# Optimization experiments

Hardware: AMD Instinct MI355X
Metric: run time of the kernel (lower is better)

## Reference

```python
import jax, jax.numpy as jnp
import numpy as np

D_MODEL = 1024
HEADS = 16
D_K = D_MODEL // HEADS
D_FF = 4096
EPS = 1e-5


def _layernorm(x, gamma, beta):
    mu = jnp.mean(x, axis=-1, keepdims=True)
    var = jnp.var(x, axis=-1, keepdims=True)
    return (x - mu) * jax.lax.rsqrt(var + EPS) * gamma + beta


def setup_inputs() -> dict:
    key = jax.random.key(0)
    ks = jax.random.split(key, 8)
    s = 0.02
    return {
        "x": jax.random.normal(ks[0], (4, 2048, D_MODEL), dtype=jnp.float32),
        "wq": jax.random.normal(ks[1], (D_MODEL, D_MODEL), dtype=jnp.float32) * s,
        "wk": jax.random.normal(ks[2], (D_MODEL, D_MODEL), dtype=jnp.float32) * s,
        "wv": jax.random.normal(ks[3], (D_MODEL, D_MODEL), dtype=jnp.float32) * s,
        "wo": jax.random.normal(ks[4], (D_MODEL, D_MODEL), dtype=jnp.float32) * s,
        "w1": jax.random.normal(ks[5], (D_MODEL, D_FF), dtype=jnp.float32) * s,
        "b1": jnp.zeros((D_FF,), dtype=jnp.float32),
        "w2": jax.random.normal(ks[6], (D_FF, D_MODEL), dtype=jnp.float32) * s,
        "b2": jnp.zeros((D_MODEL,), dtype=jnp.float32),
        "g1": jnp.ones((D_MODEL,), dtype=jnp.float32),
        "be1": jnp.zeros((D_MODEL,), dtype=jnp.float32),
        "g2": jnp.ones((D_MODEL,), dtype=jnp.float32),
        "be2": jnp.zeros((D_MODEL,), dtype=jnp.float32),
    }


def reference(x, wq, wk, wv, wo, w1, b1, w2, b2, g1, be1, g2, be2):
    B, S, D = x.shape
    # --- multi-head self-attention (dropout = identity at eval) ---
    q = (x @ wq).reshape(B, S, HEADS, D_K).transpose(0, 2, 1, 3)  # [B,H,S,dk]
    k = (x @ wk).reshape(B, S, HEADS, D_K).transpose(0, 2, 1, 3)
    v = (x @ wv).reshape(B, S, HEADS, D_K).transpose(0, 2, 1, 3)
    scores = jnp.einsum("bhqd,bhkd->bhqk", q, k) / jnp.sqrt(jnp.float32(D_K))
    attn = jax.nn.softmax(scores, axis=-1)
    ctx = jnp.einsum("bhqk,bhkd->bhqd", attn, v)
    ctx = ctx.transpose(0, 2, 1, 3).reshape(B, S, D)
    attn_out = ctx @ wo
    # --- add & norm 1 ---
    h = _layernorm(x + attn_out, g1, be1)
    # --- FFN ---
    ffn = jax.nn.relu(h @ w1 + b1) @ w2 + b2
    # --- add & norm 2 ---
    return _layernorm(h + ffn, g2, be2)
```

## Files before the change

kernel.cpp:

```cpp
#include <hip/hip_runtime.h>
#include <hip/hip_bf16.h>


typedef float  floatx2  __attribute__((ext_vector_type(2)));
typedef float  floatx4  __attribute__((ext_vector_type(4)));
typedef float  floatx16 __attribute__((ext_vector_type(16)));
typedef short  shortx8  __attribute__((ext_vector_type(8)));
typedef short  shortx4  __attribute__((ext_vector_type(4)));
typedef int    intx4    __attribute__((ext_vector_type(4)));
typedef unsigned uintx2 __attribute__((ext_vector_type(2)));

__device__ __forceinline__ short f2bs(float f) {
    union { float f; unsigned u; } a; a.f = f;
    unsigned r = a.u + 0x7fffu + ((a.u >> 16) & 1u);
    return (short)(r >> 16);
}

__device__ __forceinline__ float fexp2(float x) {
#if __has_builtin(__builtin_amdgcn_exp2f)
    return __builtin_amdgcn_exp2f(x);
#else
    return __expf(0.6931471805599453f * x);
#endif
}

__device__ __forceinline__ void lane32swap(unsigned& a, unsigned& b) {
#if __has_builtin(__builtin_amdgcn_permlane32_swap)
    uintx2 r = __builtin_amdgcn_permlane32_swap(a, b, false, false);
    a = r[0]; b = r[1];
#else
    int hl = (threadIdx.x & 63) >> 5;
    unsigned ta = (unsigned)__shfl_xor((int)a, 32);
    unsigned tb = (unsigned)__shfl_xor((int)b, 32);
    unsigned na = hl ? tb : a;
    unsigned nb = hl ? b : ta;
    a = na; b = nb;
#endif
}

__device__ __forceinline__ void gload16(const short* g, short* l) {
    __builtin_amdgcn_global_load_lds(
        (const __attribute__((address_space(1))) void*)g,
        (__attribute__((address_space(3))) void*)l,
        16, 0, 0);
}

#define WAITV(n) asm volatile("s_waitcnt vmcnt(" #n ")" ::: "memory")
#define FENCE    asm volatile("" ::: "memory")

__device__ __forceinline__ void trans_tile(const float* __restrict__ in,
                                           short* __restrict__ out,
                                           int N, int K, int k0, int n0,
                                           short (*t)[68]) {
    const int tid = threadIdx.x;
    const int r = tid >> 4, c4 = (tid & 15) * 4;
#pragma unroll
    for (int i = 0; i < 4; ++i) {
        int k = r + i * 16;
        floatx4 v = *(const floatx4*)(in + (size_t)(k0 + k) * N + n0 + c4);
        shortx4 s;
#pragma unroll
        for (int j = 0; j < 4; ++j) s[j] = f2bs(v[j]);
        *(shortx4*)(&t[k][c4]) = s;
    }
    __syncthreads();
#pragma unroll
    for (int i = 0; i < 4; ++i) {
        int n = r + i * 16;
        shortx4 s;
#pragma unroll
        for (int j = 0; j < 4; ++j) s[j] = t[c4 + j][n];
        *(shortx4*)(out + (size_t)(n0 + n) * K + k0 + c4) = s;
    }
}

__global__ __launch_bounds__(256) void prep_kernel(
    const float* __restrict__ wq, const float* __restrict__ wk,
    const float* __restrict__ wv, const float* __restrict__ wo,
    const float* __restrict__ w1, const float* __restrict__ w2,
    const float* __restrict__ x,
    short* wqt, short* wkt, short* wvt, short* wot,
    short* w1t, short* w2t, short* xb)
{
    __shared__ __align__(16) short t[64][68];
    const int bid = blockIdx.x;
    if (bid < 1024) {
        const int widx = bid >> 8, local = bid & 255;
        const float* in = widx == 0 ? wq : widx == 1 ? wk : widx == 2 ? wv : wo;
        short* out = widx == 0 ? wqt : widx == 1 ? wkt : widx == 2 ? wvt : wot;
        trans_tile(in, out, 1024, 1024, (local & 15) * 64, (local >> 4) * 64, t);
    } else if (bid < 2048) {
        const int local = bid - 1024;
        trans_tile(w1, w1t, 4096, 1024, (local & 15) * 64, (local >> 4) * 64, t);
    } else if (bid < 3072) {
        const int local = bid - 2048;
        trans_tile(w2, w2t, 1024, 4096, (local & 63) * 64, (local >> 6) * 64, t);
    } else {
        const int local = bid - 3072;
#pragma unroll
        for (int j = 0; j < 4; ++j) {
            int i = local * 1024 + j * 256 + threadIdx.x;
            floatx4 v = *(const floatx4*)(x + (size_t)i * 4);
            shortx4 o;
            o[0] = f2bs(v[0]); o[1] = f2bs(v[1]); o[2] = f2bs(v[2]); o[3] = f2bs(v[3]);
            *(shortx4*)(xb + (size_t)i * 4) = o;
        }
    }
}

template<int EPI, int BN>
__global__ __launch_bounds__(512, 2) void gemm256(
    const short* __restrict__ A, const short* __restrict__ Bt, const int K, const int N,
    short* __restrict__ outb, float* __restrict__ outf,
    const float* __restrict__ bias, const float* __restrict__ resf)
{
    constexpr int BUFSZ = 16384 + BN * 64;
    constexpr int NF = BN / 64;
    constexpr int NBUF = (BN == 128) ? 3 : 2;
    __shared__ __align__(16) short Ls[NBUF * BUFSZ];
    const int tid = threadIdx.x;
    const int w = tid >> 6, lane = tid & 63;
    const int quad = lane >> 4, l16 = lane & 15;
    const int wm = w >> 2, wn = w & 3;
    const int bx = blockIdx.x, by = blockIdx.y;

    const int srow = w * 16 + (lane >> 3);
    const int uc0 = ((lane & 7) ^ ((lane >> 4) & 7)) * 8;
    const int uc1 = ((lane & 7) ^ (((lane >> 4) + 4) & 7)) * 8;
    const short* aS0 = A  + (size_t)(by * 256 + srow) * K + uc0;
    const short* aS1 = A  + (size_t)(by * 256 + srow + 8) * K + uc1;
    const short* bS0 = Bt + (size_t)(bx * BN + srow) * K + uc0;
    const short* bS1 = Bt + (size_t)(bx * BN + srow + 8) * K + uc1;
    const size_t hK = (size_t)128 * K;
    const int wsl = w * 1024;

    const int rswz = (l16 >> 1) & 7;
    const int ru0 = (quad ^ rswz) * 8;
    const int ru1 = ((4 + quad) ^ rswz) * 8;
    const int aRd = (wm * 64 + l16) * 64;
    const int bRd = (wn * 32 + l16) * 64;

    floatx4 acc[8][NF] = {};
    shortx8 af[4][2], blo[2][2], bhi[2][2];

#define S_A0(buf, kc) { short* p = Ls + (buf) * BUFSZ + wsl;         gload16(aS0 + (kc), p);      gload16(aS1 + (kc), p + 512);      FENCE; }
#define S_A1(buf, kc) { short* p = Ls + (buf) * BUFSZ + 8192 + wsl;  gload16(aS0 + hK + (kc), p); gload16(aS1 + hK + (kc), p + 512); FENCE; }
#define S_B0(buf, kc) { short* p = Ls + (buf) * BUFSZ + 16384 + wsl; gload16(bS0 + (kc), p);      gload16(bS1 + (kc), p + 512);      FENCE; }
#define S_B1(buf, kc) { short* p = Ls + (buf) * BUFSZ + 24576 + wsl; gload16(bS0 + hK + (kc), p); gload16(bS1 + hK + (kc), p + 512); FENCE; }
#define MF(a, b, c) c = __builtin_amdgcn_mfma_f32_16x16x32_bf16(a, b, c, 0, 0, 0)

#define RD_ALO(Ab) {                                                      \
_Pragma("unroll")                                                         \
        for (int mf = 0; mf < 4; ++mf) {                                  \
            af[mf][0] = *(const shortx8*)((Ab) + aRd + mf * 1024 + ru0);  \
            af[mf][1] = *(const shortx8*)((Ab) + aRd + mf * 1024 + ru1);  \
        } }
#define RD_AHI(Ab) {                                                      \
_Pragma("unroll")                                                         \
        for (int mf = 0; mf < 4; ++mf) {                                  \
            af[mf][0] = *(const shortx8*)((Ab) + aRd + 8192 + mf * 1024 + ru0); \
            af[mf][1] = *(const shortx8*)((Ab) + aRd + 8192 + mf * 1024 + ru1); \
        } }
#define RD_BLO(Bb) {                                                      \
_Pragma("unroll")                                                         \
        for (int nf = 0; nf < 2; ++nf) {                                  \
            blo[nf][0] = *(const shortx8*)((Bb) + bRd + nf * 1024 + ru0); \
            blo[nf][1] = *(const shortx8*)((Bb) + bRd + nf * 1024 + ru1); \
        } }
#define MFMA_LO { __builtin_amdgcn_s_setprio(1);                          \
_Pragma("unroll")                                                         \
        for (int mf = 0; mf < 4; ++mf)                                    \
_Pragma("unroll")                                                         \
            for (int nf = 0; nf < 2; ++nf) {                              \
                MF(af[mf][0], blo[nf][0], acc[mf][nf]);                   \
                MF(af[mf][1], blo[nf][1], acc[mf][nf]);                   \
            }                                                             \
        __builtin_amdgcn_s_setprio(0); }
#define MFMA_HI { __builtin_amdgcn_s_setprio(1);                          \
_Pragma("unroll")                                                         \
        for (int mf = 0; mf < 4; ++mf)                                    \
_Pragma("unroll")                                                         \
            for (int nf = 0; nf < 2; ++nf) {                              \
                MF(af[mf][0], blo[nf][0], acc[4 + mf][nf]);               \
                MF(af[mf][1], blo[nf][1], acc[4 + mf][nf]);               \
            }                                                             \
        __builtin_amdgcn_s_setprio(0); }

    const int NT = K >> 6;

    if constexpr (BN == 256) {
        S_A0(0, 0) S_B0(0, 0) S_B1(0, 0) S_A1(0, 0)
        for (int t = 0; t < NT - 1; ++t) {
            const int rb = t & 1, wbuf = rb ^ 1, kc = (t + 1) * 64;
            const short* Ab = Ls + rb * BUFSZ;
            const short* Bb = Ab + 16384;
            WAITV(4); __builtin_amdgcn_s_barrier(); FENCE;
            RD_ALO(Ab) RD_BLO(Bb)
            S_A0(wbuf, kc)
            MFMA_LO
            WAITV(4); __builtin_amdgcn_s_barrier(); FENCE;
#pragma unroll
            for (int nf = 0; nf < 2; ++nf) {
                bhi[nf][0] = *(const shortx8*)(Bb + bRd + 8192 + nf * 1024 + ru0);
                bhi[nf][1] = *(const shortx8*)(Bb + bRd + 8192 + nf * 1024 + ru1);
            }
            S_B0(wbuf, kc)
            __builtin_amdgcn_s_setprio(1);
#pragma unroll
            for (int mf = 0; mf < 4; ++mf)
#pragma unroll
                for (int nf = 0; nf < 2; ++nf) {
                    MF(af[mf][0], bhi[nf][0], acc[mf][2 + nf]);
                    MF(af[mf][1], bhi[nf][1], acc[mf][2 + nf]);
                }
            __builtin_amdgcn_s_setprio(0);
            WAITV(4); __builtin_amdgcn_s_barrier(); FENCE;
            RD_AHI(Ab)
            S_B1(wbuf, kc)
            MFMA_HI
            S_A1(wbuf, kc)
            __builtin_amdgcn_s_setprio(1);
#pragma unroll
            for (int mf = 0; mf < 4; ++mf)
#pragma unroll
                for (int nf = 0; nf < 2; ++nf) {
                    MF(af[mf][0], bhi[nf][0], acc[4 + mf][2 + nf]);
                    MF(af[mf][1], bhi[nf][1], acc[4 + mf][2 + nf]);
                }
            __builtin_amdgcn_s_setprio(0);
        }
        {
            const int rb = (NT - 1) & 1;
            const short* Ab = Ls + rb * BUFSZ;
            const short* Bb = Ab + 16384;
            WAITV(4); __builtin_amdgcn_s_barrier(); FENCE;
            RD_ALO(Ab) RD_BLO(Bb)
            MFMA_LO
            WAITV(2); __builtin_amdgcn_s_barrier(); FENCE;
#pragma unroll
            for (int nf = 0; nf < 2; ++nf) {
                bhi[nf][0] = *(const shortx8*)(Bb + bRd + 8192 + nf * 1024 + ru0);
                bhi[nf][1] = *(const shortx8*)(Bb + bRd + 8192 + nf * 1024 + ru1);
            }
            __builtin_amdgcn_s_setprio(1);
#pragma unroll
            for (int mf = 0; mf < 4; ++mf)
#pragma unroll
                for (int nf = 0; nf < 2; ++nf) {
                    MF(af[mf][0], bhi[nf][0], acc[mf][2 + nf]);
                    MF(af[mf][1], bhi[nf][1], acc[mf][2 + nf]);
                }
            __builtin_amdgcn_s_setprio(0);
            WAITV(0); __builtin_amdgcn_s_barrier(); FENCE;
            RD_AHI(Ab)
            __builtin_amdgcn_s_setprio(1);
#pragma unroll
            for (int mf = 0; mf < 4; ++mf)
#pragma unroll
                for (int nf = 0; nf < 2; ++nf) {
                    MF(af[mf][0], blo[nf][0], acc[4 + mf][nf]);
                    MF(af[mf][1], blo[nf][1], acc[4 + mf][nf]);
                    MF(af[mf][0], bhi[nf][0], acc[4 + mf][2 + nf]);
                    MF(af[mf][1], bhi[nf][1], acc[4 + mf][2 + nf]);
                }
            __builtin_amdgcn_s_setprio(0);
        }
    } else {
        S_A0(0, 0) S_B0(0, 0) S_A1(0, 0)
        S_A0(1, 64) S_B0(1, 64) S_A1(1, 64)
        for (int t = 0; t < NT - 2; ++t) {
            const int rb = t % 3, pb = (t + 2) % 3, kc = (t + 2) * 64;
            const short* Ab = Ls + rb * BUFSZ;
            const short* Bb = Ab + 16384;
            WAITV(8); __builtin_amdgcn_s_barrier(); FENCE;
            RD_ALO(Ab) RD_BLO(Bb)
            S_A0(pb, kc)
            MFMA_LO
            WAITV(8); __builtin_amdgcn_s_barrier(); FENCE;
            RD_AHI(Ab)
            S_B0(pb, kc) S_A1(pb, kc)
            MFMA_HI
        }
        {
            const int rb = (NT - 2) % 3;
            const short* Ab = Ls + rb * BUFSZ;
            const short* Bb = Ab + 16384;
            WAITV(8); __builtin_amdgcn_s_barrier(); FENCE;
            RD_ALO(Ab) RD_BLO(Bb)
            MFMA_LO
            WAITV(6); __builtin_amdgcn_s_barrier(); FENCE;
            RD_AHI(Ab)
            MFMA_HI
        }
        {
            const int rb = (NT - 1) % 3;
            const short* Ab = Ls + rb * BUFSZ;
            const short* Bb = Ab + 16384;
            WAITV(2); __builtin_amdgcn_s_barrier(); FENCE;
            RD_ALO(Ab) RD_BLO(Bb)
            MFMA_LO
            WAITV(0); __builtin_amdgcn_s_barrier(); FENCE;
            RD_AHI(Ab)
            MFMA_HI
        }
    }

#pragma unroll
    for (int mf = 0; mf < 8; ++mf) {
        const int grow0 = by * 256 + (mf >> 2) * 128 + wm * 64 + (mf & 3) * 16 + quad * 4;
#pragma unroll
        for (int nf = 0; nf < NF; ++nf) {
            int gcol;
            if constexpr (BN == 256)
                gcol = bx * 256 + (nf >> 1) * 128 + wn * 32 + (nf & 1) * 16 + l16;
            else
                gcol = bx * 128 + wn * 32 + nf * 16 + l16;
            const floatx4 a = acc[mf][nf];
            if constexpr (EPI == 5) {
                const int slice = gcol >> 10, c = gcol & 1023;
                const int hh = c >> 6, d = c & 63;
                const int b = grow0 >> 11, s0 = grow0 & 2047;
                if (slice == 2) {
                    short* vt = outb + ((size_t)16 << 20);
                    shortx4 pkv;
#pragma unroll
                    for (int r = 0; r < 4; ++r) pkv[r] = f2bs(a[r]);
                    *(shortx4*)(vt + ((size_t)((b * 16 + hh) * 64 + d)) * 2048 + s0) = pkv;
                } else {
                    short* dst = slice ? (outb + ((size_t)8 << 20)) : outb;
                    float sc = slice ? 1.f : 0.125f * 1.4426950408889634f;
#pragma unroll
                    for (int r = 0; r < 4; ++r)
                        dst[(((size_t)(b * 16 + hh)) * 2048 + (s0 + r)) * 64 + d] =
                            f2bs(a[r] * sc);
                }
            } else if constexpr (EPI == 1) {
                const float bv = bias[gcol];
#pragma unroll
                for (int r = 0; r < 4; ++r) {
                    float v = fmaxf(a[r] + bv, 0.f);
                    outb[(size_t)(grow0 + r) * N + gcol] = f2bs(v);
                }
            } else if constexpr (EPI == 2) {
#pragma unroll
                for (int r = 0; r < 4; ++r)
                    outf[(size_t)(grow0 + r) * N + gcol] =
                        a[r] + resf[(size_t)(grow0 + r) * N + gcol];
            } else if constexpr (EPI == 3) {
                const float bv = bias[gcol];
#pragma unroll
                for (int r = 0; r < 4; ++r)
                    outf[(size_t)(grow0 + r) * N + gcol] =
                        a[r] + bv + resf[(size_t)(grow0 + r) * N + gcol];
            }
        }
    }
#undef S_A0
#undef S_A1
#undef S_B0
#undef S_B1
#undef MF
#undef RD_ALO
#undef RD_AHI
#undef RD_BLO
#undef MFMA_LO
#undef MFMA_HI
}

__global__ __launch_bounds__(256) void ln_kernel(
    const float* __restrict__ in, float* __restrict__ outf, short* __restrict__ outb,
    const float* __restrict__ g, const float* __restrict__ be, int writeB)
{
    __shared__ float red[8];
    const int row = blockIdx.x, tid = threadIdx.x;
    const float* p = in + (size_t)row * 1024;
    floatx4 v = *(const floatx4*)(p + tid * 4);
    float s = v[0] + v[1] + v[2] + v[3];
    float q = v[0] * v[0] + v[1] * v[1] + v[2] * v[2] + v[3] * v[3];
#pragma unroll
    for (int off = 32; off; off >>= 1) {
        s += __shfl_xor(s, off);
        q += __shfl_xor(q, off);
    }
    int w = tid >> 6, lane = tid & 63;
    if (lane == 0) { red[w] = s; red[4 + w] = q; }
    __syncthreads();
    s = red[0] + red[1] + red[2] + red[3];
    q = red[4] + red[5] + red[6] + red[7];
    float mean = s * (1.f / 1024.f);
    float var = q * (1.f / 1024.f) - mean * mean;
    float rs = rsqrtf(var + 1e-5f);
    floatx4 gv = *(const floatx4*)(g + tid * 4);
    floatx4 bv = *(const floatx4*)(be + tid * 4);
    floatx4 o4;
#pragma unroll
    for (int i = 0; i < 4; ++i) o4[i] = (v[i] - mean) * rs * gv[i] + bv[i];
    *(floatx4*)(outf + (size_t)row * 1024 + tid * 4) = o4;
    if (writeB) {
        shortx4 ob;
#pragma unroll
        for (int i = 0; i < 4; ++i) ob[i] = f2bs(o4[i]);
        *(shortx4*)(outb + (size_t)row * 1024 + tid * 4) = ob;
    }
}

__global__ __launch_bounds__(256, 4) void attn_kernel(
    const short* __restrict__ Q, const short* __restrict__ K,
    const short* __restrict__ Vt, short* __restrict__ ctx)
{
    __shared__ __align__(16) short Ls[16384];
    const int tid = threadIdx.x;
    const int q0 = blockIdx.x * 128, bh = blockIdx.y;
    const int w = tid >> 6, lane = tid & 63, l31 = lane & 31, hl = lane >> 5;
    const size_t sb = (size_t)bh * 2048 * 64;

    shortx8 qf[4];
#pragma unroll
    for (int ks = 0; ks < 4; ++ks)
        qf[ks] = *(const shortx8*)(Q + sb + (size_t)(q0 + w * 32 + l31) * 64 + ks * 16 + hl * 8);

    const int srow = w * 8 + (lane >> 3);
    const int sunit = ((lane & 7) ^ (lane >> 3)) * 8;
    const short* kSrc = K + sb + (size_t)srow * 64 + sunit;
    const short* vSrc = Vt + sb + (size_t)srow * 2048 + sunit;
    const int sdst = w * 512;

    const int kx = l31 & 7;

    floatx16 o[2] = {};
    floatx2 rsA = {0.f, 0.f}, rsB = {0.f, 0.f};
    const floatx16 z = {};

#define STAGE(buf, kv0) { \
    short* kb = Ls + (buf) * 8192 + sdst; \
    gload16(kSrc + (size_t)(kv0) * 64, kb); \
    gload16(kSrc + (size_t)(kv0) * 64 + 2048, kb + 2048); \
    gload16(vSrc + (kv0), kb + 4096); \
    gload16(vSrc + (kv0) + 65536, kb + 6144); \
    FENCE; }

#define LD_AK(B, mt, ks) (*(const shortx8*)((B) + ((mt) * 32 + l31) * 64 + ((((ks) * 2 + hl) ^ kx)) * 8))
#define LD_AV(B, mtd, mt, ksl) (*(const shortx8*)((B) + 4096 + ((mtd) * 32 + l31) * 64 + ((((mt) * 4 + (ksl) * 2 + hl) ^ kx)) * 8))

    STAGE(0, 0)

    for (int kt = 0; kt < 32; ++kt) {
        WAITV(0);
        __builtin_amdgcn_s_barrier();
        FENCE;
        if (kt < 31) STAGE((kt + 1) & 1, (kt + 1) * 64)
        const short* B = Ls + (kt & 1) * 8192;

#pragma unroll
        for (int mt = 0; mt < 2; ++mt) {
            floatx16 sc;
            __builtin_amdgcn_s_setprio(1);
            sc = __builtin_amdgcn_mfma_f32_32x32x16_bf16(LD_AK(B, mt, 0), qf[0], z, 0, 0, 0);
            sc = __builtin_amdgcn_mfma_f32_32x32x16_bf16(LD_AK(B, mt, 1), qf[1], sc, 0, 0, 0);
            sc = __builtin_amdgcn_mfma_f32_32x32x16_bf16(LD_AK(B, mt, 2), qf[2], sc, 0, 0, 0);
            sc = __builtin_amdgcn_mfma_f32_32x32x16_bf16(LD_AK(B, mt, 3), qf[3], sc, 0, 0, 0);
            __builtin_amdgcn_s_setprio(0);
            floatx2 ps2[8];
#pragma unroll
            for (int i = 0; i < 8; ++i) {
                ps2[i][0] = fexp2(sc[2 * i]);
                ps2[i][1] = fexp2(sc[2 * i + 1]);
            }
#pragma unroll
            for (int i = 0; i < 8; i += 2) { rsA += ps2[i]; rsB += ps2[i + 1]; }
            unsigned pk[8];
#pragma unroll
            for (int i = 0; i < 8; ++i) {
                union { __hip_bfloat162 h; unsigned u; } cv;
                cv.h = __float22bfloat162_rn(make_float2(ps2[i][0], ps2[i][1]));
                pk[i] = cv.u;
            }
            lane32swap(pk[0], pk[2]);
            lane32swap(pk[1], pk[3]);
            lane32swap(pk[4], pk[6]);
            lane32swap(pk[5], pk[7]);
            __builtin_amdgcn_s_setprio(1);
#pragma unroll
            for (int ksl = 0; ksl < 2; ++ksl) {
                union { unsigned i[4]; shortx8 s8; } fr;
                fr.i[0] = pk[4 * ksl];     fr.i[1] = pk[4 * ksl + 1];
                fr.i[2] = pk[4 * ksl + 2]; fr.i[3] = pk[4 * ksl + 3];
#pragma unroll
                for (int mtd = 0; mtd < 2; ++mtd)
                    o[mtd] = __builtin_amdgcn_mfma_f32_32x32x16_bf16(LD_AV(B, mtd, mt, ksl), fr.s8, o[mtd], 0, 0, 0);
            }
            __builtin_amdgcn_s_setprio(0);
        }
    }
#undef STAGE
#undef LD_AK
#undef LD_AV

    float rsum = rsA[0] + rsA[1] + rsB[0] + rsB[1];
    float tot = rsum + __shfl_xor(rsum, 32);
    float inv = 1.f / tot;

    __syncthreads();
    short* O_lds = Ls;
#pragma unroll
    for (int mtd = 0; mtd < 2; ++mtd)
#pragma unroll
        for (int g = 0; g < 4; ++g) {
            shortx4 p4;
#pragma unroll
            for (int r = 0; r < 4; ++r) p4[r] = f2bs(o[mtd][4 * g + r] * inv);
            *(shortx4*)(O_lds + (w * 32 + l31) * 72 + mtd * 32 + g * 8 + hl * 4) = p4;
        }
    __syncthreads();
    const int b = bh >> 4, head = bh & 15;
#pragma unroll
    for (int it = 0; it < 4; ++it) {
        int idx = it * 256 + tid;
        int q = idx >> 3, ch = idx & 7;
        shortx8 v = *(const shortx8*)(O_lds + q * 72 + ch * 8);
        *(shortx8*)(ctx + ((size_t)(b * 2048 + q0 + q)) * 1024 + head * 64 + ch * 8) = v;
    }
}

extern "C" void kernel_launch(void* const* d_in, const int* in_sizes, int n_in,
                              void* d_out, int out_size, void* d_ws, size_t ws_size,
                              hipStream_t stream) {
    const float* x   = (const float*)d_in[0];
    const float* wq  = (const float*)d_in[1];
    const float* wk  = (const float*)d_in[2];
    const float* wv  = (const float*)d_in[3];
    const float* wo  = (const float*)d_in[4];
    const float* w1  = (const float*)d_in[5];
    const float* b1  = (const float*)d_in[6];
    const float* w2  = (const float*)d_in[7];
    const float* b2  = (const float*)d_in[8];
    const float* g1p = (const float*)d_in[9];
    const float* be1 = (const float*)d_in[10];
    const float* g2p = (const float*)d_in[11];
    const float* be2 = (const float*)d_in[12];
    float* out = (float*)d_out;

    char* ws = (char*)d_ws;
    const size_t MB = 1ull << 20;
    short* wqt  = (short*)(ws + 0 * MB);
    short* wkt  = (short*)(ws + 2 * MB);
    short* wvt  = (short*)(ws + 4 * MB);
    short* wot  = (short*)(ws + 6 * MB);
    short* w1t  = (short*)(ws + 8 * MB);
    short* w2t  = (short*)(ws + 16 * MB);
    short* xb   = (short*)(ws + 24 * MB);
    short* Qb   = (short*)(ws + 40 * MB);
    short* Kb   = (short*)(ws + 56 * MB);
    short* Vtg  = (short*)(ws + 72 * MB);
    short* ctxb = (short*)(ws + 88 * MB);
    float* tf   = (float*)(ws + 104 * MB);
    short* hb   = (short*)(ws + 136 * MB);
    short* f1b  = (short*)(ws + 40 * MB);

    prep_kernel<<<5120, 256, 0, stream>>>(wq, wk, wv, wo, w1, w2, x,
                                          wqt, wkt, wvt, wot, w1t, w2t, xb);

    gemm256<5, 128><<<dim3(24, 32), 512, 0, stream>>>(xb, wqt, 1024, 3072, Qb, nullptr, nullptr, nullptr);
    attn_kernel<<<dim3(16, 64), 256, 0, stream>>>(Qb, Kb, Vtg, ctxb);
    gemm256<2, 128><<<dim3(8, 32), 512, 0, stream>>>(ctxb, wot, 1024, 1024, nullptr, tf, nullptr, x);
    ln_kernel<<<8192, 256, 0, stream>>>(tf, tf, hb, g1p, be1, 1);
    gemm256<1, 256><<<dim3(16, 32), 512, 0, stream>>>(hb, w1t, 1024, 4096, f1b, nullptr, b1, nullptr);
    gemm256<3, 128><<<dim3(8, 32), 512, 0, stream>>>(f1b, w2t, 4096, 1024, nullptr, out, b2, tf);
    ln_kernel<<<8192, 256, 0, stream>>>(out, out, nullptr, g2p, be2, 0);
}
```

Measured before the change: 384.1 us.

## Double attention query tile per wave and swizzle GEMM block order

The attention kernel now has each wave handle 64 query rows as two 32-row groups instead of 32, so every K/V tile staged in LDS and loaded into registers serves twice as many MFMAs. The grid is halved, occupancy is lowered to 2 blocks per CU, and LDS grows to hold the larger output staging. Separately, the GEMM kernels remap the block index to group blocks for better L2 reuse of A and B tiles. Costs are higher register pressure and fewer resident waves to hide latency, and the attention grid now has only 512 blocks.

```diff
diff --git a/kernel.cpp b/kernel.cpp
--- a/kernel.cpp
+++ b/kernel.cpp
@@ -122,7 +122,10 @@
     const int w = tid >> 6, lane = tid & 63;
     const int quad = lane >> 4, l16 = lane & 15;
     const int wm = w >> 2, wn = w & 3;
-    const int bx = blockIdx.x, by = blockIdx.y;
+    const int hsw = blockIdx.x + blockIdx.y * gridDim.x;
+    const int vv = hsw >> 3;
+    const int by = (hsw & 7) * 4 + (vv & 3);
+    const int bx = vv >> 2;
 
     const int srow = w * 16 + (lane >> 3);
     const int uc0 = ((lane & 7) ^ ((lane >> 4) & 7)) * 8;
@@ -404,20 +407,22 @@
     }
 }
 
-__global__ __launch_bounds__(256, 4) void attn_kernel(
+__global__ __launch_bounds__(256, 2) void attn_kernel(
     const short* __restrict__ Q, const short* __restrict__ K,
     const short* __restrict__ Vt, short* __restrict__ ctx)
 {
-    __shared__ __align__(16) short Ls[16384];
+    __shared__ __align__(16) short Ls[18432];
     const int tid = threadIdx.x;
-    const int q0 = blockIdx.x * 128, bh = blockIdx.y;
+    const int q0 = blockIdx.x * 256, bh = blockIdx.y;
     const int w = tid >> 6, lane = tid & 63, l31 = lane & 31, hl = lane >> 5;
     const size_t sb = (size_t)bh * 2048 * 64;
 
-    shortx8 qf[4];
-#pragma unroll
-    for (int ks = 0; ks < 4; ++ks)
-        qf[ks] = *(const shortx8*)(Q + sb + (size_t)(q0 + w * 32 + l31) * 64 + ks * 16 + hl * 8);
+    shortx8 qf[2][4];
+#pragma unroll
+    for (int qg = 0; qg < 2; ++qg)
+#pragma unroll
+        for (int ks = 0; ks < 4; ++ks)
+            qf[qg][ks] = *(const shortx8*)(Q + sb + (size_t)(q0 + w * 64 + qg * 32 + l31) * 64 + ks * 16 + hl * 8);
 
     const int srow = w * 8 + (lane >> 3);
     const int sunit = ((lane & 7) ^ (lane >> 3)) * 8;
@@ -427,8 +432,9 @@
 
     const int kx = l31 & 7;
 
-    floatx16 o[2] = {};
-    floatx2 rsA = {0.f, 0.f}, rsB = {0.f, 0.f};
+    floatx16 o[2][2] = {};
+    floatx2 rs0A = {0.f, 0.f}, rs0B = {0.f, 0.f};
+    floatx2 rs1A = {0.f, 0.f}, rs1B = {0.f, 0.f};
     const floatx16 z = {};
 
 #define STAGE(buf, kv0) { \
@@ -441,6 +447,7 @@
 
 #define LD_AK(B, mt, ks) (*(const shortx8*)((B) + ((mt) * 32 + l31) * 64 + ((((ks) * 2 + hl) ^ kx)) * 8))
 #define LD_AV(B, mtd, mt, ksl) (*(const shortx8*)((B) + 4096 + ((mtd) * 32 + l31) * 64 + ((((mt) * 4 + (ksl) * 2 + hl) ^ kx)) * 8))
+#define MFA(a, b, c) __builtin_amdgcn_mfma_f32_32x32x16_bf16(a, b, c, 0, 0, 0)
 
     STAGE(0, 0)
 
@@ -453,68 +460,99 @@
 
 #pragma unroll
         for (int mt = 0; mt < 2; ++mt) {
-            floatx16 sc;
+            shortx8 ak[4], av[2][2];
+#pragma unroll
+            for (int ks = 0; ks < 4; ++ks) ak[ks] = LD_AK(B, mt, ks);
+#pragma unroll
+            for (int ksl = 0; ksl < 2; ++ksl)
+#pragma unroll
+                for (int mtd = 0; mtd < 2; ++mtd) av[ksl][mtd] = LD_AV(B, mtd, mt, ksl);
+            floatx16 sc0, sc1;
             __builtin_amdgcn_s_setprio(1);
-            sc = __builtin_amdgcn_mfma_f32_32x32x16_bf16(LD_AK(B, mt, 0), qf[0], z, 0, 0, 0);
-            sc = __builtin_amdgcn_mfma_f32_32x32x16_bf16(LD_AK(B, mt, 1), qf[1], sc, 0, 0, 0);
-            sc = __builtin_amdgcn_mfma_f32_32x32x16_bf16(LD_AK(B, mt, 2), qf[2], sc, 0, 0, 0);
-            sc = __builtin_amdgcn_mfma_f32_32x32x16_bf16(LD_AK(B, mt, 3), qf[3], sc, 0, 0, 0);
+            sc0 = MFA(ak[0], qf[0][0], z);
+            sc0 = MFA(ak[1], qf[0][1], sc0);
+            sc0 = MFA(ak[2], qf[0][2], sc0);
+            sc0 = MFA(ak[3], qf[0][3], sc0);
+            sc1 = MFA(ak[0], qf[1][0], z);
+            sc1 = MFA(ak[1], qf[1][1], sc1);
+            sc1 = MFA(ak[2], qf[1][2], sc1);
+            sc1 = MFA(ak[3], qf[1][3], sc1);
             __builtin_amdgcn_s_setprio(0);
-            floatx2 ps2[8];
-#pragma unroll
-            for (int i = 0; i < 8; ++i) {
-                ps2[i][0] = fexp2(sc[2 * i]);
-                ps2[i][1] = fexp2(sc[2 * i + 1]);
+#pragma unroll
+            for (int qg = 0; qg < 2; ++qg) {
+                const floatx16 sc = qg ? sc1 : sc0;
+                floatx2 ps2[8];
+#pragma unroll
+                for (int i = 0; i < 8; ++i) {
+                    ps2[i][0] = fexp2(sc[2 * i]);
+                    ps2[i][1] = fexp2(sc[2 * i + 1]);
+                }
+                if (qg == 0) {
+#pragma unroll
+                    for (int i = 0; i < 8; i += 2) { rs0A += ps2[i]; rs0B += ps2[i + 1]; }
+                } else {
+#pragma unroll
+                    for (int i = 0; i < 8; i += 2) { rs1A += ps2[i]; rs1B += ps2[i + 1]; }
+                }
+                unsigned pk[8];
+#pragma unroll
+                for (int i = 0; i < 8; ++i) {
+                    union { __hip_bfloat162 h; unsigned u; } cv;
+                    cv.h = __float22bfloat162_rn(make_float2(ps2[i][0], ps2[i][1]));
+                    pk[i] = cv.u;
+                }
+                lane32swap(pk[0], pk[2]);
+                lane32swap(pk[1], pk[3]);
+                lane32swap(pk[4], pk[6]);
+                lane32swap(pk[5], pk[7]);
+                __builtin_amdgcn_s_setprio(1);
+#pragma unroll
+                for (int ksl = 0; ksl < 2; ++ksl) {
+                    union { unsigned i[4]; shortx8 s8; } fr;
+                    fr.i[0] = pk[4 * ksl];     fr.i[1] = pk[4 * ksl + 1];
+                    fr.i[2] = pk[4 * ksl + 2]; fr.i[3] = pk[4 * ksl + 3];
+#pragma unroll
+                    for (int mtd = 0; mtd < 2; ++mtd)
+                        o[qg][mtd] = MFA(av[ksl][mtd], fr.s8, o[qg][mtd]);
+                }
+                __builtin_amdgcn_s_setprio(0);
             }
-#pragma unroll
-            for (int i = 0; i < 8; i += 2) { rsA += ps2[i]; rsB += ps2[i + 1]; }
-            unsigned pk[8];
-#pragma unroll
-            for (int i = 0; i < 8; ++i) {
-                union { __hip_bfloat162 h; unsigned u; } cv;
-                cv.h = __float22bfloat162_rn(make_float2(ps2[i][0], ps2[i][1]));
-                pk[i] = cv.u;
-            }
-            lane32swap(pk[0], pk[2]);
-            lane32swap(pk[1], pk[3]);
-            lane32swap(pk[4], pk[6]);
-            lane32swap(pk[5], pk[7]);
-            __builtin_amdgcn_s_setprio(1);
-#pragma unroll
-            for (int ksl = 0; ksl < 2; ++ksl) {
-                union { unsigned i[4]; shortx8 s8; } fr;
-                fr.i[0] = pk[4 * ksl];     fr.i[1] = pk[4 * ksl + 1];
-                fr.i[2] = pk[4 * ksl + 2]; fr.i[3] = pk[4 * ksl + 3];
-#pragma unroll
-                for (int mtd = 0; mtd < 2; ++mtd)
-                    o[mtd] = __builtin_amdgcn_mfma_f32_32x32x16_bf16(LD_AV(B, mtd, mt, ksl), fr.s8, o[mtd], 0, 0, 0);
-            }
-            __builtin_amdgcn_s_setprio(0);
         }
     }
 #undef STAGE
 #undef LD_AK
 #undef LD_AV
-
-    float rsum = rsA[0] + rsA[1] + rsB[0] + rsB[1];
-    float tot = rsum + __shfl_xor(rsum, 32);
-    float inv = 1.f / tot;
+#undef MFA
+
+    float inv0, inv1;
+    {
+        float r0 = rs0A[0] + rs0A[1] + rs0B[0] + rs0B[1];
+        float t0 = r0 + __shfl_xor(r0, 32);
+        inv0 = 1.f / t0;
+        float r1 = rs1A[0] + rs1A[1] + rs1B[0] + rs1B[1];
+        float t1 = r1 + __shfl_xor(r1, 32);
+        inv1 = 1.f / t1;
+    }
 
     __syncthreads();
     short* O_lds = Ls;
 #pragma unroll
-    for (int mtd = 0; mtd < 2; ++mtd)
-#pragma unroll
-        for (int g = 0; g < 4; ++g) {
-            shortx4 p4;
-#pragma unroll
-            for (int r = 0; r < 4; ++r) p4[r] = f2bs(o[mtd][4 * g + r] * inv);
-            *(shortx4*)(O_lds + (w * 32 + l31) * 72 + mtd * 32 + g * 8 + hl * 4) = p4;
-        }
+    for (int qg = 0; qg < 2; ++qg) {
+        const float inv = qg ? inv1 : inv0;
+#pragma unroll
+        for (int mtd = 0; mtd < 2; ++mtd)
+#pragma unroll
+            for (int g = 0; g < 4; ++g) {
+                shortx4 p4;
+#pragma unroll
+                for (int r = 0; r < 4; ++r) p4[r] = f2bs(o[qg][mtd][4 * g + r] * inv);
+                *(shortx4*)(O_lds + (w * 64 + qg * 32 + l31) * 72 + mtd * 32 + g * 8 + hl * 4) = p4;
+            }
+    }
     __syncthreads();
     const int b = bh >> 4, head = bh & 15;
 #pragma unroll
-    for (int it = 0; it < 4; ++it) {
+    for (int it = 0; it < 8; ++it) {
         int idx = it * 256 + tid;
         int q = idx >> 3, ch = idx & 7;
         shortx8 v = *(const shortx8*)(O_lds + q * 72 + ch * 8);
@@ -561,7 +599,7 @@
                                           wqt, wkt, wvt, wot, w1t, w2t, xb);
 
     gemm256<5, 128><<<dim3(24, 32), 512, 0, stream>>>(xb, wqt, 1024, 3072, Qb, nullptr, nullptr, nullptr);
-    attn_kernel<<<dim3(16, 64), 256, 0, stream>>>(Qb, Kb, Vtg, ctxb);
+    attn_kernel<<<dim3(8, 64), 256, 0, stream>>>(Qb, Kb, Vtg, ctxb);
     gemm256<2, 128><<<dim3(8, 32), 512, 0, stream>>>(ctxb, wot, 1024, 1024, nullptr, tf, nullptr, x);
     ln_kernel<<<8192, 256, 0, stream>>>(tf, tf, hb, g1p, be1, 1);
     gemm256<1, 256><<<dim3(16, 32), 512, 0, stream>>>(hb, w1t, 1024, 4096, f1b, nullptr, b1, nullptr);
```

Result: faster. 356.3 us (-7.3%).

## Load K/V fragments directly from global in attention and swizzle GEMM block order

Applied to the files above, without the earlier changes.

The attention kernel drops its double-buffered LDS staging of K and V and instead has each wave load its MFMA operand fragments straight from global memory (relying on L1/L2 reuse across waves), with an occasional barrier every 8 tiles to keep waves loosely in step. This removes the LDS copy and the per-tile barriers, at the cost of redundant global/cache traffic across the four waves and exposed load latency. Separately, the GEMM remaps block indices into groups of row tiles to improve L2 reuse of A and B tiles.

```diff
diff --git a/kernel.cpp b/kernel.cpp
--- a/kernel.cpp
+++ b/kernel.cpp
@@ -122,7 +122,10 @@
     const int w = tid >> 6, lane = tid & 63;
     const int quad = lane >> 4, l16 = lane & 15;
     const int wm = w >> 2, wn = w & 3;
-    const int bx = blockIdx.x, by = blockIdx.y;
+    const int hsw = blockIdx.x + blockIdx.y * gridDim.x;
+    const int vv = hsw >> 3;
+    const int by = (hsw & 7) * 4 + (vv & 3);
+    const int bx = vv >> 2;
 
     const int srow = w * 16 + (lane >> 3);
     const int uc0 = ((lane & 7) ^ ((lane >> 4) & 7)) * 8;
@@ -408,7 +411,7 @@
     const short* __restrict__ Q, const short* __restrict__ K,
     const short* __restrict__ Vt, short* __restrict__ ctx)
 {
-    __shared__ __align__(16) short Ls[16384];
+    __shared__ __align__(16) short O_lds[128 * 72];
     const int tid = threadIdx.x;
     const int q0 = blockIdx.x * 128, bh = blockIdx.y;
     const int w = tid >> 6, lane = tid & 63, l31 = lane & 31, hl = lane >> 5;
@@ -419,89 +422,73 @@
     for (int ks = 0; ks < 4; ++ks)
         qf[ks] = *(const shortx8*)(Q + sb + (size_t)(q0 + w * 32 + l31) * 64 + ks * 16 + hl * 8);
 
-    const int srow = w * 8 + (lane >> 3);
-    const int sunit = ((lane & 7) ^ (lane >> 3)) * 8;
-    const short* kSrc = K + sb + (size_t)srow * 64 + sunit;
-    const short* vSrc = Vt + sb + (size_t)srow * 2048 + sunit;
-    const int sdst = w * 512;
-
-    const int kx = l31 & 7;
+    const short* kB = K + sb + (size_t)l31 * 64 + hl * 8;
+    const short* vB = Vt + sb + (size_t)l31 * 2048 + hl * 8;
 
     floatx16 o[2] = {};
     floatx2 rsA = {0.f, 0.f}, rsB = {0.f, 0.f};
     const floatx16 z = {};
 
-#define STAGE(buf, kv0) { \
-    short* kb = Ls + (buf) * 8192 + sdst; \
-    gload16(kSrc + (size_t)(kv0) * 64, kb); \
-    gload16(kSrc + (size_t)(kv0) * 64 + 2048, kb + 2048); \
-    gload16(vSrc + (kv0), kb + 4096); \
-    gload16(vSrc + (kv0) + 65536, kb + 6144); \
-    FENCE; }
-
-#define LD_AK(B, mt, ks) (*(const shortx8*)((B) + ((mt) * 32 + l31) * 64 + ((((ks) * 2 + hl) ^ kx)) * 8))
-#define LD_AV(B, mtd, mt, ksl) (*(const shortx8*)((B) + 4096 + ((mtd) * 32 + l31) * 64 + ((((mt) * 4 + (ksl) * 2 + hl) ^ kx)) * 8))
-
-    STAGE(0, 0)
-
-    for (int kt = 0; kt < 32; ++kt) {
-        WAITV(0);
-        __builtin_amdgcn_s_barrier();
-        FENCE;
-        if (kt < 31) STAGE((kt + 1) & 1, (kt + 1) * 64)
-        const short* B = Ls + (kt & 1) * 8192;
-
-#pragma unroll
-        for (int mt = 0; mt < 2; ++mt) {
-            floatx16 sc;
-            __builtin_amdgcn_s_setprio(1);
-            sc = __builtin_amdgcn_mfma_f32_32x32x16_bf16(LD_AK(B, mt, 0), qf[0], z, 0, 0, 0);
-            sc = __builtin_amdgcn_mfma_f32_32x32x16_bf16(LD_AK(B, mt, 1), qf[1], sc, 0, 0, 0);
-            sc = __builtin_amdgcn_mfma_f32_32x32x16_bf16(LD_AK(B, mt, 2), qf[2], sc, 0, 0, 0);
-            sc = __builtin_amdgcn_mfma_f32_32x32x16_bf16(LD_AK(B, mt, 3), qf[3], sc, 0, 0, 0);
-            __builtin_amdgcn_s_setprio(0);
-            floatx2 ps2[8];
-#pragma unroll
-            for (int i = 0; i < 8; ++i) {
-                ps2[i][0] = fexp2(sc[2 * i]);
-                ps2[i][1] = fexp2(sc[2 * i + 1]);
-            }
-#pragma unroll
-            for (int i = 0; i < 8; i += 2) { rsA += ps2[i]; rsB += ps2[i + 1]; }
-            unsigned pk[8];
-#pragma unroll
-            for (int i = 0; i < 8; ++i) {
-                union { __hip_bfloat162 h; unsigned u; } cv;
-                cv.h = __float22bfloat162_rn(make_float2(ps2[i][0], ps2[i][1]));
-                pk[i] = cv.u;
-            }
-            lane32swap(pk[0], pk[2]);
-            lane32swap(pk[1], pk[3]);
-            lane32swap(pk[4], pk[6]);
-            lane32swap(pk[5], pk[7]);
-            __builtin_amdgcn_s_setprio(1);
-#pragma unroll
-            for (int ksl = 0; ksl < 2; ++ksl) {
-                union { unsigned i[4]; shortx8 s8; } fr;
-                fr.i[0] = pk[4 * ksl];     fr.i[1] = pk[4 * ksl + 1];
-                fr.i[2] = pk[4 * ksl + 2]; fr.i[3] = pk[4 * ksl + 3];
-#pragma unroll
-                for (int mtd = 0; mtd < 2; ++mtd)
-                    o[mtd] = __builtin_amdgcn_mfma_f32_32x32x16_bf16(LD_AV(B, mtd, mt, ksl), fr.s8, o[mtd], 0, 0, 0);
-            }
-            __builtin_amdgcn_s_setprio(0);
-        }
-    }
-#undef STAGE
-#undef LD_AK
-#undef LD_AV
+#define MFA(a, b, c) __builtin_amdgcn_mfma_f32_32x32x16_bf16(a, b, c, 0, 0, 0)
+
+    for (int t = 0; t < 64; ++t) {
+        const int kvb = t * 32;
+        const short* kp = kB + kvb * 64;
+        shortx8 ak0 = *(const shortx8*)(kp);
+        shortx8 ak1 = *(const shortx8*)(kp + 16);
+        shortx8 ak2 = *(const shortx8*)(kp + 32);
+        shortx8 ak3 = *(const shortx8*)(kp + 48);
+        const short* vp = vB + kvb;
+        shortx8 av00 = *(const shortx8*)(vp);
+        shortx8 av01 = *(const shortx8*)(vp + 65536);
+        shortx8 av10 = *(const shortx8*)(vp + 16);
+        shortx8 av11 = *(const shortx8*)(vp + 16 + 65536);
+
+        floatx16 sc;
+        __builtin_amdgcn_s_setprio(1);
+        sc = MFA(ak0, qf[0], z);
+        sc = MFA(ak1, qf[1], sc);
+        sc = MFA(ak2, qf[2], sc);
+        sc = MFA(ak3, qf[3], sc);
+        __builtin_amdgcn_s_setprio(0);
+
+        floatx2 ps2[8];
+#pragma unroll
+        for (int i = 0; i < 8; ++i) {
+            ps2[i][0] = fexp2(sc[2 * i]);
+            ps2[i][1] = fexp2(sc[2 * i + 1]);
+        }
+#pragma unroll
+        for (int i = 0; i < 8; i += 2) { rsA += ps2[i]; rsB += ps2[i + 1]; }
+        unsigned pk[8];
+#pragma unroll
+        for (int i = 0; i < 8; ++i) {
+            union { __hip_bfloat162 h; unsigned u; } cv;
+            cv.h = __float22bfloat162_rn(make_float2(ps2[i][0], ps2[i][1]));
+            pk[i] = cv.u;
+        }
+        lane32swap(pk[0], pk[2]);
+        lane32swap(pk[1], pk[3]);
+        lane32swap(pk[4], pk[6]);
+        lane32swap(pk[5], pk[7]);
+        union { unsigned i[4]; shortx8 s8; } fr0, fr1;
+        fr0.i[0] = pk[0]; fr0.i[1] = pk[1]; fr0.i[2] = pk[2]; fr0.i[3] = pk[3];
+        fr1.i[0] = pk[4]; fr1.i[1] = pk[5]; fr1.i[2] = pk[6]; fr1.i[3] = pk[7];
+        __builtin_amdgcn_s_setprio(1);
+        o[0] = MFA(av00, fr0.s8, o[0]);
+        o[1] = MFA(av01, fr0.s8, o[1]);
+        o[0] = MFA(av10, fr1.s8, o[0]);
+        o[1] = MFA(av11, fr1.s8, o[1]);
+        __builtin_amdgcn_s_setprio(0);
+
+        if ((t & 7) == 7) __builtin_amdgcn_s_barrier();
+    }
+#undef MFA
 
     float rsum = rsA[0] + rsA[1] + rsB[0] + rsB[1];
     float tot = rsum + __shfl_xor(rsum, 32);
     float inv = 1.f / tot;
 
-    __syncthreads();
-    short* O_lds = Ls;
 #pragma unroll
     for (int mtd = 0; mtd < 2; ++mtd)
 #pragma unroll
```

New measurement: 502.7 us. +30.9%, slower.
